# Performance work log

Hardware: AMD Instinct MI355X
Metric: run time of the kernel (lower is better)

Reference implementation:

```python
import jax, jax.numpy as jnp
import numpy as np

B, S = 8, 2048
D_IN, D_STATE, D_OUT = 1024, 1024, 1024
H = 16
DH = D_STATE // H  # 64
N_LAYERS = 24
STD = 0.02
EPS = 1e-6


def setup_inputs() -> dict:
    key = jax.random.key(0)
    k = jax.random.split(key, 4)
    x = jax.random.normal(k[0], (B, S, D_IN), dtype=jnp.float32)
    # input_projection: Linear(D_IN, 4*D_STATE, bias=False), std=0.02
    w_in = jax.random.normal(k[1], (D_IN, 4 * D_STATE), dtype=jnp.float32) * STD
    # state_weight: [3*H, DH, DH] recurrence matrices (candidate, forget, reset)
    state_weight = jax.random.normal(k[2], (3 * H, DH, DH), dtype=jnp.float32) * STD
    # rmsnorm weight over state_size
    norm_weight = jnp.ones((D_STATE,), dtype=jnp.float32)
    # output_projection: Linear(D_STATE, D_OUT, bias=False), std scaled by sqrt(2*num_layers)
    w_out = jax.random.normal(k[3], (D_STATE, D_OUT), dtype=jnp.float32) * (STD / np.sqrt(2 * N_LAYERS))
    return {"x": x, "w_in": w_in, "state_weight": state_weight,
            "norm_weight": norm_weight, "w_out": w_out}


def _rmsnorm(x, w):
    var = jnp.mean(jnp.square(x), axis=-1, keepdims=True)
    return x * jax.lax.rsqrt(var + EPS) * w


def reference(x, w_in, state_weight, norm_weight, w_out):
    # input projection -> [B, S, 4*D_STATE]
    proj = jnp.einsum('bsi,io->bso', x, w_in)
    xg, g = jnp.split(proj, [3 * D_STATE], axis=-1)
    xi, xf, xr = jnp.split(xg, 3, axis=-1)
    # per-head views [B, S, H, DH]
    xi = xi.reshape(B, S, H, DH)
    xf = xf.reshape(B, S, H, DH)
    xr = xr.reshape(B, S, H, DH)
    W, Wf, Wr = jnp.split(state_weight, 3, axis=0)  # each [H, DH, DH]

    # scan over time: carry h [B, H, DH]
    def step(h, inp):
        xi_t, xf_t, xr_t = inp  # each [B, H, DH]
        r = jax.nn.sigmoid(xr_t + jnp.einsum('bhd,hde->bhe', h, Wr))
        f = jax.nn.sigmoid(xf_t + jnp.einsum('bhd,hde->bhe', h, Wf))
        c = jnp.tanh(xi_t + jnp.einsum('bhd,hde->bhe', r * h, W))
        h_new = f * h + (1.0 - f) * c
        return h_new, h_new

    h0 = jnp.zeros((B, H, DH), dtype=x.dtype)
    xs = (jnp.swapaxes(xi, 0, 1), jnp.swapaxes(xf, 0, 1), jnp.swapaxes(xr, 0, 1))
    _, hs = jax.lax.scan(step, h0, xs)  # hs: [S, B, H, DH]
    h_seq = jnp.swapaxes(hs, 0, 1).reshape(B, S, D_STATE)

    # gated output: h * silu(g), rmsnorm, output projection
    y = h_seq * jax.nn.silu(g)
    y = _rmsnorm(y, norm_weight)
    return jnp.einsum('bsd,do->bso', y, w_out)
```

## Files before the change

### kernel.cpp

```cpp
#include <hip/hip_runtime.h>
#include <hip/hip_bf16.h>
#include <math.h>

typedef __hip_bfloat16 bf16;

#define B_      8
#define S_      2048
#define DIN     1024
#define DSTATE  1024
#define H_      16
#define DH_     64
#define PROJ4   4096

#define BARRIER_LGKM() asm volatile("s_waitcnt lgkmcnt(0)\n\ts_barrier" ::: "memory")

__device__ __forceinline__ unsigned short f2bf(float f) {
    unsigned int x = __float_as_uint(f);
    x += 0x7FFFu + ((x >> 16) & 1u);
    return (unsigned short)(x >> 16);
}

__device__ __forceinline__ float4 load4(const float* p) { return *(const float4*)p; }
__device__ __forceinline__ float4 load4(const bf16* p) {
    uint2 u = *(const uint2*)p;
    float4 r;
    r.x = __uint_as_float((u.x & 0xFFFFu) << 16);
    r.y = __uint_as_float(u.x & 0xFFFF0000u);
    r.z = __uint_as_float((u.y & 0xFFFFu) << 16);
    r.w = __uint_as_float(u.y & 0xFFFF0000u);
    return r;
}
__device__ __forceinline__ void store4(float* p, float4 v) { *(float4*)p = v; }
__device__ __forceinline__ void store4(bf16* p, float4 v) {
    uint2 u;
    u.x = (unsigned int)f2bf(v.x) | ((unsigned int)f2bf(v.y) << 16);
    u.y = (unsigned int)f2bf(v.z) | ((unsigned int)f2bf(v.w) << 16);
    *(uint2*)p = u;
}

typedef __attribute__((ext_vector_type(8))) short bf16x8;
typedef __attribute__((ext_vector_type(4))) float f32x4;

__global__ __launch_bounds__(256) void cast_x_kernel(const float* __restrict__ src,
                                                     bf16* __restrict__ dst, int n8) {
    int i = blockIdx.x * 256 + threadIdx.x;
    if (i >= n8) return;
    const float* p = src + (size_t)i * 8;
    bf16* q = dst + (size_t)i * 8;
    store4(q, load4(p));
    store4(q + 4, load4(p + 4));
}

__global__ __launch_bounds__(256) void transpose_cast_kernel(
        const float* __restrict__ src, bf16* __restrict__ dst, int R, int C) {
    __shared__ short t64[64][65];
    const int tid = threadIdx.x;
    const int r0 = blockIdx.y * 64;
    const int c0 = blockIdx.x * 64;
    const int rr = tid >> 4;
    const int c4 = (tid & 15) * 4;

    #pragma unroll
    for (int p = 0; p < 4; ++p) {
        int r = rr + p * 16;
        float4 v = load4(src + (size_t)(r0 + r) * C + c0 + c4);
        t64[r][c4 + 0] = (short)f2bf(v.x);
        t64[r][c4 + 1] = (short)f2bf(v.y);
        t64[r][c4 + 2] = (short)f2bf(v.z);
        t64[r][c4 + 3] = (short)f2bf(v.w);
    }
    __syncthreads();
    #pragma unroll
    for (int p = 0; p < 4; ++p) {
        int cc = rr + p * 16;
        unsigned int s0 = (unsigned short)t64[c4 + 0][cc] |
                          ((unsigned int)(unsigned short)t64[c4 + 1][cc] << 16);
        unsigned int s1 = (unsigned short)t64[c4 + 2][cc] |
                          ((unsigned int)(unsigned short)t64[c4 + 3][cc] << 16);
        uint2 u = make_uint2(s0, s1);
        *(uint2*)&dst[(size_t)(c0 + cc) * R + r0 + c4] = u;
    }
}

template <typename TC>
__global__ __launch_bounds__(256) void gemm_bt(const bf16* __restrict__ A,
                                               const bf16* __restrict__ BT,
                                               TC* __restrict__ C,
                                               int N, int K, int lda, int ldb) {
    __shared__ short As[128 * 40];
    __shared__ short Bs[128 * 40];

    const int tid = threadIdx.x;
    const int m0 = blockIdx.y * 128;
    const int n0 = blockIdx.x * 128;

    const int row = tid >> 1;
    const int ks  = (tid & 1) * 16;

    const int wid = tid >> 6;
    const int wx = wid & 1, wy = wid >> 1;
    const int lane = tid & 63;
    const int c16 = lane & 15;
    const int quad = lane >> 4;

    const bf16* Ap = A + (size_t)(m0 + row) * lda + ks;
    const bf16* Bp = BT + (size_t)(n0 + row) * ldb + ks;

    f32x4 acc[4][4];
    #pragma unroll
    for (int i = 0; i < 4; ++i)
        #pragma unroll
        for (int j = 0; j < 4; ++j) acc[i][j] = (f32x4){0.f, 0.f, 0.f, 0.f};

    uint4 ra0 = *(const uint4*)Ap;
    uint4 ra1 = *(const uint4*)(Ap + 8);
    uint4 rb0 = *(const uint4*)Bp;
    uint4 rb1 = *(const uint4*)(Bp + 8);

    for (int k0 = 0; k0 < K; k0 += 32) {
        __syncthreads();
        *(uint4*)&As[row * 40 + ks]     = ra0;
        *(uint4*)&As[row * 40 + ks + 8] = ra1;
        *(uint4*)&Bs[row * 40 + ks]     = rb0;
        *(uint4*)&Bs[row * 40 + ks + 8] = rb1;
        __syncthreads();

        if (k0 + 32 < K) {
            ra0 = *(const uint4*)(Ap + k0 + 32);
            ra1 = *(const uint4*)(Ap + k0 + 40);
            rb0 = *(const uint4*)(Bp + k0 + 32);
            rb1 = *(const uint4*)(Bp + k0 + 40);
        }

        bf16x8 af[4], bfr[4];
        #pragma unroll
        for (int mt = 0; mt < 4; ++mt)
            af[mt] = *(const bf16x8*)&As[(wy * 64 + mt * 16 + c16) * 40 + quad * 8];
        #pragma unroll
        for (int nt = 0; nt < 4; ++nt)
            bfr[nt] = *(const bf16x8*)&Bs[(wx * 64 + nt * 16 + c16) * 40 + quad * 8];

        #pragma unroll
        for (int mt = 0; mt < 4; ++mt)
            #pragma unroll
            for (int nt = 0; nt < 4; ++nt)
                acc[mt][nt] = __builtin_amdgcn_mfma_f32_16x16x32_bf16(
                    af[mt], bfr[nt], acc[mt][nt], 0, 0, 0);
    }

    #pragma unroll
    for (int mt = 0; mt < 4; ++mt) {
        #pragma unroll
        for (int r = 0; r < 4; ++r) {
            int rowc = m0 + wy * 64 + mt * 16 + quad * 4 + r;
            TC* cp = C + (size_t)rowc * N + n0 + wx * 64;
            #pragma unroll
            for (int nt = 0; nt < 4; ++nt)
                cp[nt * 16 + c16] = (TC)acc[mt][nt][r];
        }
    }
}

__device__ __forceinline__ float lane_bcast(float v, int lane) {
    return __int_as_float(__builtin_amdgcn_readlane(__float_as_int(v), lane));
}

#define RPT16(M) M(0) M(1) M(2) M(3) M(4) M(5) M(6) M(7) \
                 M(8) M(9) M(10) M(11) M(12) M(13) M(14) M(15)

__global__ __launch_bounds__(256, 1)
__attribute__((amdgpu_waves_per_eu(1, 2)))
void recur_kernel(bf16* __restrict__ proj, const float* __restrict__ sw) {
    const int tid = threadIdx.x;
    const int e = tid & 63;
    const int w = __builtin_amdgcn_readfirstlane(tid >> 6);
    const int d0 = w << 4;
    const int bh = blockIdx.x;
    const int b = bh >> 4;
    const int h = bh & 15;

    __shared__ float2 part_rf[4][64];
    __shared__ float  part_c[4][64];
    __shared__ char lds_force[60 * 1024];
    asm volatile("" :: "v"((unsigned int)(size_t)lds_force));

    const float* Wc_p = sw + (size_t)h * 4096 + (size_t)d0 * 64 + e;
    const float* Wf_p = Wc_p + (size_t)16 * 4096;
    const float* Wr_p = Wc_p + (size_t)32 * 4096;

    #define DECLW(i) float wc##i, wf##i, wr##i;
    RPT16(DECLW)
    #undef DECLW
    #define LOADW(i) wc##i = Wc_p[(i) * 64]; \
                     wf##i = Wf_p[(i) * 64]; \
                     wr##i = Wr_p[(i) * 64];
    RPT16(LOADW)
    #undef LOADW
    #define PINW(i) asm volatile("" : "+v"(wc##i), "+v"(wf##i), "+v"(wr##i));
    RPT16(PINW)
    #undef PINW

    bf16* xi_p = proj + (size_t)b * S_ * PROJ4 + h * 64 + e;

    f32x4 rxi, rxf, rxr;
    #define PRELOAD(U) { const bf16* p = xi_p + (size_t)(U) * PROJ4; \
        rxi[U] = __bfloat162float(p[0]); \
        rxf[U] = __bfloat162float(p[1024]); \
        rxr[U] = __bfloat162float(p[2048]); }
    PRELOAD(0) PRELOAD(1) PRELOAD(2) PRELOAD(3)
    #undef PRELOAD

    float hreg = 0.0f;

    const bf16* ld = xi_p + (size_t)4 * PROJ4;
    bf16*       st = xi_p;

    #define P1T(i, A) { float hb = lane_bcast(hreg, d0 + (i)); \
        aR##A = fmaf(hb, wr##i, aR##A); \
        aF##A = fmaf(hb, wf##i, aF##A); }
    #define P2T(i, A) { float qb = lane_bcast(rh, d0 + (i)); \
        aC##A = fmaf(qb, wc##i, aC##A); }

    #define STEP(U, REFILL) { \
        float xi0 = rxi[U], xf0 = rxf[U], xr0 = rxr[U]; \
        if (REFILL) { \
            const bf16* p = ld + (size_t)(U) * PROJ4; \
            rxi[U] = __bfloat162float(p[0]); \
            rxf[U] = __bfloat162float(p[1024]); \
            rxr[U] = __bfloat162float(p[2048]); \
        } \
        float aR0 = 0.f, aR1 = 0.f, aF0 = 0.f, aF1 = 0.f; \
        P1T(0,0)  P1T(1,1)  P1T(2,0)  P1T(3,1) \
        P1T(4,0)  P1T(5,1)  P1T(6,0)  P1T(7,1) \
        P1T(8,0)  P1T(9,1)  P1T(10,0) P1T(11,1) \
        P1T(12,0) P1T(13,1) P1T(14,0) P1T(15,1) \
        part_rf[w][e] = make_float2(aR0 + aR1, aF0 + aF1); \
        BARRIER_LGKM(); \
        float2 p0 = part_rf[0][e], p1 = part_rf[1][e]; \
        float2 p2 = part_rf[2][e], p3 = part_rf[3][e]; \
        float sr = xr0 + (p0.x + p1.x) + (p2.x + p3.x); \
        float sf = xf0 + (p0.y + p1.y) + (p2.y + p3.y); \
        float r = 1.f / (1.f + __expf(-sr)); \
        float f = 1.f / (1.f + __expf(-sf)); \
        float rh = r * hreg; \
        float aC0 = 0.f, aC1 = 0.f; \
        P2T(0,0)  P2T(1,1)  P2T(2,0)  P2T(3,1) \
        P2T(4,0)  P2T(5,1)  P2T(6,0)  P2T(7,1) \
        P2T(8,0)  P2T(9,1)  P2T(10,0) P2T(11,1) \
        P2T(12,0) P2T(13,1) P2T(14,0) P2T(15,1) \
        part_c[w][e] = aC0 + aC1; \
        BARRIER_LGKM(); \
        float sc = xi0 + (part_c[0][e] + part_c[1][e]) \
                       + (part_c[2][e] + part_c[3][e]); \
        sc = fminf(fmaxf(sc, -15.f), 15.f); \
        float ex = __expf(-2.f * sc); \
        float cc = (1.f - ex) / (1.f + ex); \
        hreg = f * hreg + (1.f - f) * cc; \
        if (w == (U)) st[(size_t)(U) * PROJ4] = __float2bfloat16(hreg); \
    }

    for (int t0 = 0; t0 < S_ - 4; t0 += 4) {
        STEP(0, 1) STEP(1, 1) STEP(2, 1) STEP(3, 1)
        ld += (size_t)4 * PROJ4;
        st += (size_t)4 * PROJ4;
    }
    STEP(0, 0) STEP(1, 0) STEP(2, 0) STEP(3, 0)

    #undef STEP
    #undef P1T
    #undef P2T
}

__global__ __launch_bounds__(256) void gate_norm_kernel(bf16* __restrict__ proj,
                                                        const float* __restrict__ nw) {
    const int row = blockIdx.x;
    const int tid = threadIdx.x;
    __shared__ float red[4];

    bf16* hp = proj + (size_t)row * PROJ4;
    const bf16* gp = hp + 3 * DSTATE;

    float4 hv = load4(hp + tid * 4);
    float4 gv = load4(gp + tid * 4);

    float v0 = hv.x * (gv.x / (1.f + __expf(-gv.x)));
    float v1 = hv.y * (gv.y / (1.f + __expf(-gv.y)));
    float v2 = hv.z * (gv.z / (1.f + __expf(-gv.z)));
    float v3 = hv.w * (gv.w / (1.f + __expf(-gv.w)));

    float ss = v0 * v0 + v1 * v1 + v2 * v2 + v3 * v3;
    #pragma unroll
    for (int mask = 32; mask >= 1; mask >>= 1)
        ss += __shfl_xor(ss, mask, 64);

    const int wid = tid >> 6;
    if ((tid & 63) == 0) red[wid] = ss;
    __syncthreads();
    float tot = red[0] + red[1] + red[2] + red[3];
    float scale = rsqrtf(tot * (1.0f / (float)DSTATE) + 1e-6f);

    float4 nv = *(const float4*)(nw + tid * 4);
    float4 y;
    y.x = v0 * scale * nv.x;
    y.y = v1 * scale * nv.y;
    y.z = v2 * scale * nv.z;
    y.w = v3 * scale * nv.w;
    store4(hp + tid * 4, y);
}

extern "C" void kernel_launch(void* const* d_in, const int* in_sizes, int n_in,
                              void* d_out, int out_size, void* d_ws, size_t ws_size,
                              hipStream_t stream) {
    const float* x     = (const float*)d_in[0];
    const float* w_in  = (const float*)d_in[1];
    const float* sw    = (const float*)d_in[2];
    const float* nw    = (const float*)d_in[3];
    const float* w_out = (const float*)d_in[4];
    float* out = (float*)d_out;

    char* ws = (char*)d_ws;
    bf16* proj   = (bf16*)ws;
    bf16* xb     = (bf16*)(ws + 134217728);
    bf16* w_inT  = (bf16*)(ws + 134217728 + 33554432);
    bf16* w_outT = (bf16*)(ws + 134217728 + 33554432 + 8388608);

    cast_x_kernel<<<(B_ * S_ * DIN / 8 + 255) / 256, 256, 0, stream>>>(x, xb,
                                                                B_ * S_ * DIN / 8);
    transpose_cast_kernel<<<dim3(PROJ4 / 64, DIN / 64), 256, 0, stream>>>(
        w_in, w_inT, DIN, PROJ4);
    transpose_cast_kernel<<<dim3(DSTATE / 64, DSTATE / 64), 256, 0, stream>>>(
        w_out, w_outT, DSTATE, DSTATE);

    gemm_bt<bf16><<<dim3(PROJ4 / 128, (B_ * S_) / 128), 256, 0, stream>>>(
        xb, w_inT, proj, PROJ4, DIN, DIN, DIN);

    recur_kernel<<<128, 256, 0, stream>>>(proj, sw);

    gate_norm_kernel<<<B_ * S_, 256, 0, stream>>>(proj, nw);

    gemm_bt<float><<<dim3(DSTATE / 128, (B_ * S_) / 128), 256, 0, stream>>>(
        proj, w_outT, out, DSTATE, DSTATE, PROJ4, DSTATE);
}
```

Measured before the change: 1.482 ms.

## Process two batch sequences per block in recurrence kernel to amortize barriers

Each recurrence block now advances two independent batch sequences for the same head, sharing the register-resident recurrence weights and the per-step LDS barriers. The grid is halved to 64 blocks. The goal is to hide the latency of lane broadcasts, barriers and transcendentals by interleaving two independent dependency chains. The trade-off is fewer active CUs and higher register pressure.

```diff
diff --git a/kernel.cpp b/kernel.cpp
--- a/kernel.cpp
+++ b/kernel.cpp
@@ -175,13 +175,13 @@
     const int e = tid & 63;
     const int w = __builtin_amdgcn_readfirstlane(tid >> 6);
     const int d0 = w << 4;
-    const int bh = blockIdx.x;
-    const int b = bh >> 4;
-    const int h = bh & 15;
-
-    __shared__ float2 part_rf[4][64];
-    __shared__ float  part_c[4][64];
-    __shared__ char lds_force[60 * 1024];
+    const int bid = blockIdx.x;
+    const int b0 = bid >> 4;
+    const int h = bid & 15;
+
+    __shared__ float2 part_rf[2][4][64];
+    __shared__ float  part_c[2][4][64];
+    __shared__ char lds_force[56 * 1024];
     asm volatile("" :: "v"((unsigned int)(size_t)lds_force));
 
     const float* Wc_p = sw + (size_t)h * 4096 + (size_t)d0 * 64 + e;
@@ -200,75 +200,115 @@
     RPT16(PINW)
     #undef PINW
 
-    bf16* xi_p = proj + (size_t)b * S_ * PROJ4 + h * 64 + e;
-
-    f32x4 rxi, rxf, rxr;
-    #define PRELOAD(U) { const bf16* p = xi_p + (size_t)(U) * PROJ4; \
-        rxi[U] = __bfloat162float(p[0]); \
-        rxf[U] = __bfloat162float(p[1024]); \
-        rxr[U] = __bfloat162float(p[2048]); }
+    bf16* xiA = proj + (size_t)b0 * S_ * PROJ4 + h * 64 + e;
+    bf16* xiB = proj + (size_t)(b0 + 4) * S_ * PROJ4 + h * 64 + e;
+
+    f32x4 rxiA, rxfA, rxrA, rxiB, rxfB, rxrB;
+    #define PRELOAD(U) { const bf16* p = xiA + (size_t)(U) * PROJ4; \
+        rxiA[U] = __bfloat162float(p[0]); \
+        rxfA[U] = __bfloat162float(p[1024]); \
+        rxrA[U] = __bfloat162float(p[2048]); \
+        const bf16* q = xiB + (size_t)(U) * PROJ4; \
+        rxiB[U] = __bfloat162float(q[0]); \
+        rxfB[U] = __bfloat162float(q[1024]); \
+        rxrB[U] = __bfloat162float(q[2048]); }
     PRELOAD(0) PRELOAD(1) PRELOAD(2) PRELOAD(3)
     #undef PRELOAD
 
-    float hreg = 0.0f;
-
-    const bf16* ld = xi_p + (size_t)4 * PROJ4;
-    bf16*       st = xi_p;
-
-    #define P1T(i, A) { float hb = lane_bcast(hreg, d0 + (i)); \
-        aR##A = fmaf(hb, wr##i, aR##A); \
-        aF##A = fmaf(hb, wf##i, aF##A); }
-    #define P2T(i, A) { float qb = lane_bcast(rh, d0 + (i)); \
-        aC##A = fmaf(qb, wc##i, aC##A); }
+    float hA = 0.0f, hB = 0.0f;
+
+    const bf16* ldA = xiA + (size_t)4 * PROJ4;
+    bf16*       stA = xiA;
+    const bf16* ldB = xiB + (size_t)4 * PROJ4;
+    bf16*       stB = xiB;
+
+    #define P1TA(i, X) { float hb = lane_bcast(hA, d0 + (i)); \
+        aRA##X = fmaf(hb, wr##i, aRA##X); \
+        aFA##X = fmaf(hb, wf##i, aFA##X); }
+    #define P1TB(i, X) { float hb = lane_bcast(hB, d0 + (i)); \
+        aRB##X = fmaf(hb, wr##i, aRB##X); \
+        aFB##X = fmaf(hb, wf##i, aFB##X); }
+    #define P2TA(i, X) { float qb = lane_bcast(rhA, d0 + (i)); \
+        aCA##X = fmaf(qb, wc##i, aCA##X); }
+    #define P2TB(i, X) { float qb = lane_bcast(rhB, d0 + (i)); \
+        aCB##X = fmaf(qb, wc##i, aCB##X); }
+    #define APPLY16(M) \
+        M(0,0)  M(1,1)  M(2,0)  M(3,1)  M(4,0)  M(5,1)  M(6,0)  M(7,1) \
+        M(8,0)  M(9,1)  M(10,0) M(11,1) M(12,0) M(13,1) M(14,0) M(15,1)
 
     #define STEP(U, REFILL) { \
-        float xi0 = rxi[U], xf0 = rxf[U], xr0 = rxr[U]; \
+        float xiA0 = rxiA[U], xfA0 = rxfA[U], xrA0 = rxrA[U]; \
+        float xiB0 = rxiB[U], xfB0 = rxfB[U], xrB0 = rxrB[U]; \
         if (REFILL) { \
-            const bf16* p = ld + (size_t)(U) * PROJ4; \
-            rxi[U] = __bfloat162float(p[0]); \
-            rxf[U] = __bfloat162float(p[1024]); \
-            rxr[U] = __bfloat162float(p[2048]); \
+            const bf16* p = ldA + (size_t)(U) * PROJ4; \
+            rxiA[U] = __bfloat162float(p[0]); \
+            rxfA[U] = __bfloat162float(p[1024]); \
+            rxrA[U] = __bfloat162float(p[2048]); \
+            const bf16* q = ldB + (size_t)(U) * PROJ4; \
+            rxiB[U] = __bfloat162float(q[0]); \
+            rxfB[U] = __bfloat162float(q[1024]); \
+            rxrB[U] = __bfloat162float(q[2048]); \
         } \
-        float aR0 = 0.f, aR1 = 0.f, aF0 = 0.f, aF1 = 0.f; \
-        P1T(0,0)  P1T(1,1)  P1T(2,0)  P1T(3,1) \
-        P1T(4,0)  P1T(5,1)  P1T(6,0)  P1T(7,1) \
-        P1T(8,0)  P1T(9,1)  P1T(10,0) P1T(11,1) \
-        P1T(12,0) P1T(13,1) P1T(14,0) P1T(15,1) \
-        part_rf[w][e] = make_float2(aR0 + aR1, aF0 + aF1); \
+        float aRA0 = 0.f, aRA1 = 0.f, aFA0 = 0.f, aFA1 = 0.f; \
+        float aRB0 = 0.f, aRB1 = 0.f, aFB0 = 0.f, aFB1 = 0.f; \
+        APPLY16(P1TA) \
+        APPLY16(P1TB) \
+        part_rf[0][w][e] = make_float2(aRA0 + aRA1, aFA0 + aFA1); \
+        part_rf[1][w][e] = make_float2(aRB0 + aRB1, aFB0 + aFB1); \
         BARRIER_LGKM(); \
-        float2 p0 = part_rf[0][e], p1 = part_rf[1][e]; \
-        float2 p2 = part_rf[2][e], p3 = part_rf[3][e]; \
-        float sr = xr0 + (p0.x + p1.x) + (p2.x + p3.x); \
-        float sf = xf0 + (p0.y + p1.y) + (p2.y + p3.y); \
-        float r = 1.f / (1.f + __expf(-sr)); \
-        float f = 1.f / (1.f + __expf(-sf)); \
-        float rh = r * hreg; \
-        float aC0 = 0.f, aC1 = 0.f; \
-        P2T(0,0)  P2T(1,1)  P2T(2,0)  P2T(3,1) \
-        P2T(4,0)  P2T(5,1)  P2T(6,0)  P2T(7,1) \
-        P2T(8,0)  P2T(9,1)  P2T(10,0) P2T(11,1) \
-        P2T(12,0) P2T(13,1) P2T(14,0) P2T(15,1) \
-        part_c[w][e] = aC0 + aC1; \
+        float2 a0 = part_rf[0][0][e], a1 = part_rf[0][1][e]; \
+        float2 a2 = part_rf[0][2][e], a3 = part_rf[0][3][e]; \
+        float2 b0v = part_rf[1][0][e], b1v = part_rf[1][1][e]; \
+        float2 b2v = part_rf[1][2][e], b3v = part_rf[1][3][e]; \
+        float srA = xrA0 + (a0.x + a1.x) + (a2.x + a3.x); \
+        float sfA = xfA0 + (a0.y + a1.y) + (a2.y + a3.y); \
+        float srB = xrB0 + (b0v.x + b1v.x) + (b2v.x + b3v.x); \
+        float sfB = xfB0 + (b0v.y + b1v.y) + (b2v.y + b3v.y); \
+        float rA = 1.f / (1.f + __expf(-srA)); \
+        float fA = 1.f / (1.f + __expf(-sfA)); \
+        float rB = 1.f / (1.f + __expf(-srB)); \
+        float fB = 1.f / (1.f + __expf(-sfB)); \
+        float rhA = rA * hA; \
+        float rhB = rB * hB; \
+        float aCA0 = 0.f, aCA1 = 0.f, aCB0 = 0.f, aCB1 = 0.f; \
+        APPLY16(P2TA) \
+        APPLY16(P2TB) \
+        part_c[0][w][e] = aCA0 + aCA1; \
+        part_c[1][w][e] = aCB0 + aCB1; \
         BARRIER_LGKM(); \
-        float sc = xi0 + (part_c[0][e] + part_c[1][e]) \
-                       + (part_c[2][e] + part_c[3][e]); \
-        sc = fminf(fmaxf(sc, -15.f), 15.f); \
-        float ex = __expf(-2.f * sc); \
-        float cc = (1.f - ex) / (1.f + ex); \
-        hreg = f * hreg + (1.f - f) * cc; \
-        if (w == (U)) st[(size_t)(U) * PROJ4] = __float2bfloat16(hreg); \
+        float scA = xiA0 + (part_c[0][0][e] + part_c[0][1][e]) \
+                         + (part_c[0][2][e] + part_c[0][3][e]); \
+        float scB = xiB0 + (part_c[1][0][e] + part_c[1][1][e]) \
+                         + (part_c[1][2][e] + part_c[1][3][e]); \
+        scA = fminf(fmaxf(scA, -15.f), 15.f); \
+        scB = fminf(fmaxf(scB, -15.f), 15.f); \
+        float exA = __expf(-2.f * scA); \
+        float exB = __expf(-2.f * scB); \
+        float ccA = (1.f - exA) / (1.f + exA); \
+        float ccB = (1.f - exB) / (1.f + exB); \
+        hA = fA * hA + (1.f - fA) * ccA; \
+        hB = fB * hB + (1.f - fB) * ccB; \
+        if (w == (U)) { \
+            stA[(size_t)(U) * PROJ4] = __float2bfloat16(hA); \
+            stB[(size_t)(U) * PROJ4] = __float2bfloat16(hB); \
+        } \
     }
 
     for (int t0 = 0; t0 < S_ - 4; t0 += 4) {
         STEP(0, 1) STEP(1, 1) STEP(2, 1) STEP(3, 1)
-        ld += (size_t)4 * PROJ4;
-        st += (size_t)4 * PROJ4;
+        ldA += (size_t)4 * PROJ4;
+        stA += (size_t)4 * PROJ4;
+        ldB += (size_t)4 * PROJ4;
+        stB += (size_t)4 * PROJ4;
     }
     STEP(0, 0) STEP(1, 0) STEP(2, 0) STEP(3, 0)
 
     #undef STEP
-    #undef P1T
-    #undef P2T
+    #undef P1TA
+    #undef P1TB
+    #undef P2TA
+    #undef P2TB
+    #undef APPLY16
 }
 
 __global__ __launch_bounds__(256) void gate_norm_kernel(bf16* __restrict__ proj,
@@ -334,7 +374,7 @@
     gemm_bt<bf16><<<dim3(PROJ4 / 128, (B_ * S_) / 128), 256, 0, stream>>>(
         xb, w_inT, proj, PROJ4, DIN, DIN, DIN);
 
-    recur_kernel<<<128, 256, 0, stream>>>(proj, sw);
+    recur_kernel<<<64, 256, 0, stream>>>(proj, sw);
 
     gate_norm_kernel<<<B_ * S_, 256, 0, stream>>>(proj, nw);
 
```

After: 2.444 ms. 1.65x slower.
